# Kernel optimization log

Measured on AMD Instinct MI355X. Metric: run time of the kernel, lower is better.

## Reference

```python
import jax, jax.numpy as jnp
import numpy as np

D_MODEL = 1024
NUM_HEADS = 16
HEAD_DIM = D_MODEL // NUM_HEADS
NUM_KERNELS = 21


def tisa_bias(amp, off, sharp, seq_len):
    # amp/off/sharp: (H, K). Returns (H, L, L) translation-invariant bias.
    # Evaluate on the 2L-1 distinct relative distances, then gather (Toeplitz).
    d = jnp.arange(-(seq_len - 1), seq_len, dtype=amp.dtype)  # (2L-1,)
    # (H, K, 2L-1) -> sum over kernels -> (H, 2L-1)
    scores = jnp.sum(
        amp[:, :, None]
        * jnp.exp(-jnp.abs(sharp)[:, :, None] * (d[None, None, :] - off[:, :, None]) ** 2),
        axis=1,
    )
    i = jnp.arange(seq_len)
    rel_idx = i[None, :] - i[:, None] + (seq_len - 1)  # (L, L) in [0, 2L-2]
    return scores[:, rel_idx]  # (H, L, L)


def setup_inputs() -> dict:
    key = jax.random.key(0)
    ks = jax.random.split(key, 9)
    B, L = 4, 1024
    s = 0.02
    return {
        "x_q": jax.random.normal(ks[0], (B, L, D_MODEL), dtype=jnp.float32),
        "x_kv": jax.random.normal(ks[1], (B, L, D_MODEL), dtype=jnp.float32),
        "Wq": jax.random.normal(ks[2], (D_MODEL, D_MODEL), dtype=jnp.float32) * s,
        "Wm": jax.random.normal(ks[3], (D_MODEL, 2 * D_MODEL), dtype=jnp.float32) * s,
        "Wg": jax.random.normal(ks[4], (D_MODEL, 2 * D_MODEL), dtype=jnp.float32) * s,
        "bg": jnp.zeros((2 * D_MODEL,), dtype=jnp.float32),
        "tisa_amp": jax.random.normal(ks[5], (NUM_HEADS, NUM_KERNELS), dtype=jnp.float32) * 0.1,
        "tisa_off": jax.random.uniform(ks[6], (NUM_HEADS, NUM_KERNELS), dtype=jnp.float32, minval=-512.0, maxval=512.0),
        "tisa_sharp": jax.random.uniform(ks[7], (NUM_HEADS, NUM_KERNELS), dtype=jnp.float32, minval=1e-4, maxval=0.05),
    }


def reference(x_q, x_kv, Wq, Wm, Wg, bg, tisa_amp, tisa_off, tisa_sharp):
    B, Lq, _ = x_q.shape
    Lkv = x_kv.shape[1]
    H, Dh = NUM_HEADS, HEAD_DIM

    q = (x_q @ Wq).reshape(B, Lq, H, Dh).transpose(0, 2, 1, 3)        # (B,H,Lq,Dh)
    mem = (x_kv @ Wm)                                                 # (B,Lkv,2D)
    k = mem[..., :D_MODEL].reshape(B, Lkv, H, Dh).transpose(0, 2, 1, 3)
    v = mem[..., D_MODEL:].reshape(B, Lkv, H, Dh).transpose(0, 2, 1, 3)

    scale = 1.0 / jnp.sqrt(jnp.asarray(Dh, dtype=q.dtype))
    scores = jnp.einsum("bhqd,bhkd->bhqk", q, k) * scale              # (B,H,Lq,Lkv)
    scores = scores + tisa_bias(tisa_amp, tisa_off, tisa_sharp, Lkv)[None]
    weights = jax.nn.softmax(scores, axis=-1)

    attn = jnp.einsum("bhqk,bhkd->bhqd", weights, v)                  # (B,H,Lq,Dh)
    attn = attn.transpose(0, 2, 1, 3).reshape(B, Lq, D_MODEL)

    g = attn @ Wg + bg                                                # (B,Lq,2D)
    a, b = g[..., :D_MODEL], g[..., D_MODEL:]
    return a * jax.nn.sigmoid(b)
```

## Files before the change

kernel.cpp:

```cpp
#include <hip/hip_runtime.h>
#include <cstdint>
#include <cstddef>

typedef __attribute__((ext_vector_type(8))) short bf16x8;
typedef __attribute__((ext_vector_type(4))) float f32x4;

#define LOG2E 1.44269504f

__device__ __forceinline__ unsigned short f2bf(float x) {
  unsigned int u = __float_as_uint(x);
  u += 0x7FFFu + ((u >> 16) & 1u);
  return (unsigned short)(u >> 16);
}
__device__ __forceinline__ unsigned short f2bf_trunc(float x) {
  return (unsigned short)(__float_as_uint(x) >> 16);
}

__device__ __forceinline__ void gload_lds16(const void* g, void* l) {
  __builtin_amdgcn_global_load_lds(
      (const __attribute__((address_space(1))) unsigned int*)g,
      (__attribute__((address_space(3))) unsigned int*)l, 16, 0, 0);
}


__global__ void preproc(const float* __restrict__ x_q, const float* __restrict__ x_kv,
                        const float* __restrict__ Wq, const float* __restrict__ Wm,
                        const float* __restrict__ Wg,
                        const float* __restrict__ amp, const float* __restrict__ off,
                        const float* __restrict__ sharp,
                        ushort4* __restrict__ bXq, ushort4* __restrict__ bXkv,
                        unsigned short* __restrict__ dWq, unsigned short* __restrict__ dWm,
                        unsigned short* __restrict__ dWg, float* __restrict__ tab) {
  __shared__ float tile[32][33];
  const int blk = blockIdx.x;
  if (blk < 8192) {
    int i = blk * 256 + threadIdx.x;
    float4 v;
    ushort4* d;
    if (i < (1 << 20)) { v = ((const float4*)x_q)[i]; d = bXq + i; }
    else { int j = i - (1 << 20); v = ((const float4*)x_kv)[j]; d = bXkv + j; }
    ushort4 o;
    o.x = f2bf(v.x); o.y = f2bf(v.y); o.z = f2bf(v.z); o.w = f2bf(v.w);
    *d = o;
  } else if (blk < 14336) {
    int idx = blk - 8192;
    int z = idx >> 11, rem = idx & 2047;
    int bx = rem & 63, by = rem >> 6;
    const float* src = z == 0 ? Wq : (z == 1 ? Wm : Wg);
    unsigned short* dst = z == 0 ? dWq : (z == 1 ? dWm : dWg);
    int N = z == 0 ? 1024 : 2048;
    int nb = bx * 32, kb = by * 32;
    if (nb >= N) return;
    int tx = threadIdx.x & 31, ty = threadIdx.x >> 5;
#pragma unroll
    for (int r = ty; r < 32; r += 8)
      tile[r][tx] = src[(size_t)(kb + r) * N + nb + tx];
    __syncthreads();
#pragma unroll
    for (int r = ty; r < 32; r += 8)
      dst[(size_t)(nb + r) * 1024 + kb + tx] = f2bf(tile[tx][r]);
  } else {
    int h = blk - 14336;
    for (int idx = threadIdx.x; idx < 2047; idx += 256) {
      float d = (float)(idx - 1023);
      float acc = 0.f;
#pragma unroll
      for (int k = 0; k < 21; ++k) {
        float dd = d - off[h * 21 + k];
        acc += amp[h * 21 + k] * __expf(-fabsf(sharp[h * 21 + k]) * dd * dd);
      }
      tab[h * 2047 + idx] = acc * LOG2E;
    }
  }
}


__global__ __launch_bounds__(512, 2)
void qkv_gemm(const unsigned short* __restrict__ Xq,
              const unsigned short* __restrict__ Xkv,
              const unsigned short* __restrict__ WqT,
              const unsigned short* __restrict__ WmT,
              unsigned short* __restrict__ qbuf,
              unsigned short* __restrict__ kbuf,
              unsigned short* __restrict__ vtbuf) {
  __shared__ unsigned short sA[3][256 * 32];
  __shared__ unsigned short sB[3][256 * 32];
  const int y = blockIdx.y;
  const bool isQ = y < 4;
  const int ntile = (isQ ? y : y - 4) << 8;
  const unsigned short* A = isQ ? Xq : Xkv;
  const unsigned short* Bp = (isQ ? WqT : WmT) + (size_t)ntile * 1024;
  const int mtile = blockIdx.x << 8;
  const int t = threadIdx.x, lane = t & 63, w = t >> 6;
  const int wm = w >> 2, wn = w & 3;
  const int c = lane & 15, g = lane >> 4;

  const int sr = t >> 2;
  const int sch = (t & 3) ^ ((sr >> 1) & 3);
  const unsigned short* aP0 = A + (size_t)(mtile + sr) * 1024 + sch * 8;
  const unsigned short* aP1 = aP0 + 128 * 1024;
  const unsigned short* bP0 = Bp + (size_t)sr * 1024 + sch * 8;
  const unsigned short* bP1 = bP0 + 128 * 1024;
  const int lw = t * 8;

  bf16x8 cur0[4], pend[4], infl[4];
  cur0[0] = *(const bf16x8*)(aP0);
  cur0[1] = *(const bf16x8*)(aP1);
  cur0[2] = *(const bf16x8*)(bP0);
  cur0[3] = *(const bf16x8*)(bP1);
  pend[0] = *(const bf16x8*)(aP0 + 32);
  pend[1] = *(const bf16x8*)(aP1 + 32);
  pend[2] = *(const bf16x8*)(bP0 + 32);
  pend[3] = *(const bf16x8*)(bP1 + 32);
  *(bf16x8*)&sA[0][lw]        = cur0[0];
  *(bf16x8*)&sA[0][4096 + lw] = cur0[1];
  *(bf16x8*)&sB[0][lw]        = cur0[2];
  *(bf16x8*)&sB[0][4096 + lw] = cur0[3];
  asm volatile("s_waitcnt lgkmcnt(0)" ::: "memory");
  __builtin_amdgcn_sched_barrier(0);
  asm volatile("s_barrier" ::: "memory");

  const int gx = (g ^ ((c >> 1) & 3)) * 8;
  const int aoff = (wm * 128 + c) * 32 + gx;
  const int boff = (wn * 64 + c) * 32 + gx;

  f32x4 acc[8][4] = {};
  int s0 = 0, s1 = 1, s2 = 2;

  for (int kt = 0; kt < 32; ++kt) {
    if (kt + 2 < 32) {
      const int ko = (kt + 2) * 32;
      infl[0] = *(const bf16x8*)(aP0 + ko);
      infl[1] = *(const bf16x8*)(aP1 + ko);
      infl[2] = *(const bf16x8*)(bP0 + ko);
      infl[3] = *(const bf16x8*)(bP1 + ko);
    }

    const unsigned short* sAp = &sA[s0][0];
    const unsigned short* sBc = &sB[s0][0];
    bf16x8 bfr[4], a0[4], a1[4];
#pragma unroll
    for (int j = 0; j < 4; ++j) bfr[j] = *(const bf16x8*)&sBc[boff + j * 512];
#pragma unroll
    for (int i = 0; i < 4; ++i) a0[i] = *(const bf16x8*)&sAp[aoff + i * 512];
#pragma unroll
    for (int i = 0; i < 4; ++i) a1[i] = *(const bf16x8*)&sAp[aoff + 2048 + i * 512];

    __builtin_amdgcn_s_setprio(1);
#pragma unroll
    for (int i = 0; i < 4; ++i)
#pragma unroll
      for (int j = 0; j < 4; ++j)
        acc[i][j] = __builtin_amdgcn_mfma_f32_16x16x32_bf16(a0[i], bfr[j], acc[i][j], 0, 0, 0);
#pragma unroll
    for (int i = 0; i < 4; ++i)
#pragma unroll
      for (int j = 0; j < 4; ++j)
        acc[i + 4][j] = __builtin_amdgcn_mfma_f32_16x16x32_bf16(a1[i], bfr[j], acc[i + 4][j], 0, 0, 0);
    __builtin_amdgcn_s_setprio(0);

    if (kt + 1 < 32) {
      *(bf16x8*)&sA[s1][lw]        = pend[0];
      *(bf16x8*)&sA[s1][4096 + lw] = pend[1];
      *(bf16x8*)&sB[s1][lw]        = pend[2];
      *(bf16x8*)&sB[s1][4096 + lw] = pend[3];
    }
#pragma unroll
    for (int q = 0; q < 4; ++q) pend[q] = infl[q];

    asm volatile("s_waitcnt lgkmcnt(0)" ::: "memory");
    __builtin_amdgcn_sched_barrier(0);
    asm volatile("s_barrier" ::: "memory");
    __builtin_amdgcn_sched_barrier(0);

    int tmp = s0; s0 = s1; s1 = s2; s2 = tmp;
  }

  const int row0 = mtile + wm * 128 + (g << 2);
  const int col0 = ntile + wn * 64 + c;
  if (isQ) {
#pragma unroll
    for (int i = 0; i < 8; ++i)
#pragma unroll
      for (int j = 0; j < 4; ++j) {
        int r = row0 + i * 16, cl = col0 + j * 16;
#pragma unroll
        for (int ri = 0; ri < 4; ++ri)
          qbuf[(size_t)(r + ri) * 1024 + cl] = f2bf(acc[i][j][ri] * (0.125f * LOG2E));
      }
  } else if (ntile < 1024) {
#pragma unroll
    for (int i = 0; i < 8; ++i)
#pragma unroll
      for (int j = 0; j < 4; ++j) {
        int r = row0 + i * 16, cl = col0 + j * 16;
#pragma unroll
        for (int ri = 0; ri < 4; ++ri)
          kbuf[(size_t)(r + ri) * 1024 + cl] = f2bf(acc[i][j][ri]);
      }
  } else {
#pragma unroll
    for (int i = 0; i < 8; ++i)
#pragma unroll
      for (int j = 0; j < 4; ++j) {
        int r = row0 + i * 16, cl = col0 + j * 16;
        int d = cl - 1024;
        int hh = d >> 6, dh = d & 63;
        int bb2 = r >> 10, ll = r & 1023;
        ushort4 pk;
        pk.x = f2bf(acc[i][j][0]);
        pk.y = f2bf(acc[i][j][1]);
        pk.z = f2bf(acc[i][j][2]);
        pk.w = f2bf(acc[i][j][3]);
        *(ushort4*)&vtbuf[((size_t)((bb2 * 16 + hh) * 64 + dh) << 10) + ll] = pk;
      }
  }
}


__global__ __launch_bounds__(512)
void attn_kernel(const unsigned short* __restrict__ qbuf,
                 const unsigned short* __restrict__ kbuf,
                 const unsigned short* __restrict__ vtbuf,
                 const float* __restrict__ biasTab,
                 unsigned short* __restrict__ attnb) {
  const int h = blockIdx.x & 15, b = blockIdx.x >> 4, qt = blockIdx.y;
  __shared__ unsigned short sK[2][64 * 64];
  __shared__ unsigned short sV[3][64 * 64];
  __shared__ unsigned short sP[2][128 * 64];
  __shared__ float sLsum[2][128];
  const int t = threadIdx.x, lane = t & 63, w = t >> 6;
  const int c = lane & 15, g = lane >> 4;
  const int rg = w >> 1, cg = w & 1;

  const int r = t >> 3, ch = (t & 7) ^ (r & 7);

  const unsigned short* qsrc = qbuf + (size_t)(b * 1024 + qt * 128) * 1024 + h * 64;
  const unsigned short* ksrc = kbuf + (size_t)(b * 1024) * 1024 + h * 64;
  const unsigned short* vsrc = vtbuf + (size_t)((b * 16 + h) * 64) * 1024;

  unsigned short* sQ = &sP[0][0];
  gload_lds16(qsrc + (size_t)r * 1024 + ch * 8, &sQ[t * 8]);
  gload_lds16(qsrc + (size_t)(r + 64) * 1024 + ch * 8, &sQ[4096 + t * 8]);
  gload_lds16(ksrc + (size_t)r * 1024 + ch * 8, &sK[0][t * 8]);
  gload_lds16(vsrc + (size_t)r * 1024 + ch * 8, &sV[0][t * 8]);

  const float* bb = biasTab + h * 2047 + 1023 + cg * 32 + c - qt * 128 - rg * 32 - g * 4;

  float bc[2][2][4];
#pragma unroll
  for (int rf = 0; rf < 2; ++rf)
#pragma unroll
    for (int nf = 0; nf < 2; ++nf)
#pragma unroll
      for (int ri = 0; ri < 4; ++ri)
        bc[rf][nf][ri] = bb[(nf - rf) * 16 - ri];

  __syncthreads();

  bf16x8 aq[2][2];
#pragma unroll
  for (int rf = 0; rf < 2; ++rf) {
    int row = rg * 32 + rf * 16 + c;
#pragma unroll
    for (int ks = 0; ks < 2; ++ks)
      aq[rf][ks] = *(const bf16x8*)&sQ[row * 64 + (((ks * 4 + g) ^ (row & 7)) * 8)];
  }
  __syncthreads();

  f32x4 o[2][2] = {};
  float lsum[2][4] = {};

  int vcur = 0, vnx = 1;
  for (int kv = 0; kv < 16; ++kv) {
    const int cur = kv & 1;

    f32x4 s[2][2];
#pragma unroll
    for (int rf = 0; rf < 2; ++rf)
#pragma unroll
      for (int nf = 0; nf < 2; ++nf)
#pragma unroll
        for (int ri = 0; ri < 4; ++ri)
          s[rf][nf][ri] = bc[rf][nf][ri];

    if (kv + 1 < 16) {
      gload_lds16(ksrc + (size_t)((kv + 1) * 64 + r) * 1024 + ch * 8, &sK[1 - cur][t * 8]);
      gload_lds16(vsrc + (size_t)r * 1024 + (kv + 1) * 64 + ch * 8, &sV[vnx][t * 8]);
      const float* bk = bb + (kv + 1) * 64;
#pragma unroll
      for (int rf = 0; rf < 2; ++rf)
#pragma unroll
        for (int nf = 0; nf < 2; ++nf)
#pragma unroll
          for (int ri = 0; ri < 4; ++ri)
            bc[rf][nf][ri] = bk[(nf - rf) * 16 - ri];
    }

#pragma unroll
    for (int nf = 0; nf < 2; ++nf) {
      int krow = cg * 32 + nf * 16 + c;
      bf16x8 k0 = *(const bf16x8*)&sK[cur][krow * 64 + (((g) ^ (krow & 7)) * 8)];
      bf16x8 k1 = *(const bf16x8*)&sK[cur][krow * 64 + (((4 + g) ^ (krow & 7)) * 8)];
#pragma unroll
      for (int rf = 0; rf < 2; ++rf) {
        s[rf][nf] = __builtin_amdgcn_mfma_f32_16x16x32_bf16(aq[rf][0], k0, s[rf][nf], 0, 0, 0);
        s[rf][nf] = __builtin_amdgcn_mfma_f32_16x16x32_bf16(aq[rf][1], k1, s[rf][nf], 0, 0, 0);
      }
    }

#pragma unroll
    for (int rf = 0; rf < 2; ++rf)
#pragma unroll
      for (int nf = 0; nf < 2; ++nf)
#pragma unroll
        for (int ri = 0; ri < 4; ++ri) {
          float e = exp2f(s[rf][nf][ri]);
          lsum[rf][ri] += e;
          int prow = rg * 32 + rf * 16 + g * 4 + ri;
          int chunk = cg * 4 + nf * 2 + (c >> 3);
          sP[cur][prow * 64 + ((chunk ^ (prow & 7)) * 8) + (c & 7)] = f2bf_trunc(e);
        }
    __syncthreads();

    bf16x8 ap[2][2];
#pragma unroll
    for (int rf = 0; rf < 2; ++rf) {
      int row = rg * 32 + rf * 16 + c;
#pragma unroll
      for (int ks = 0; ks < 2; ++ks)
        ap[rf][ks] = *(const bf16x8*)&sP[cur][row * 64 + (((ks * 4 + g) ^ (row & 7)) * 8)];
    }
#pragma unroll
    for (int df = 0; df < 2; ++df) {
      int vrow = cg * 32 + df * 16 + c;
      bf16x8 v0 = *(const bf16x8*)&sV[vcur][vrow * 64 + (((g) ^ (vrow & 7)) * 8)];
      bf16x8 v1 = *(const bf16x8*)&sV[vcur][vrow * 64 + (((4 + g) ^ (vrow & 7)) * 8)];
#pragma unroll
      for (int rf = 0; rf < 2; ++rf) {
        o[rf][df] = __builtin_amdgcn_mfma_f32_16x16x32_bf16(ap[rf][0], v0, o[rf][df], 0, 0, 0);
        o[rf][df] = __builtin_amdgcn_mfma_f32_16x16x32_bf16(ap[rf][1], v1, o[rf][df], 0, 0, 0);
      }
    }
    vcur = vnx;
    vnx = (vnx == 2) ? 0 : vnx + 1;
  }

#pragma unroll
  for (int off = 1; off < 16; off <<= 1)
#pragma unroll
    for (int rf = 0; rf < 2; ++rf)
#pragma unroll
      for (int ri = 0; ri < 4; ++ri)
        lsum[rf][ri] += __shfl_xor(lsum[rf][ri], off, 64);
  if (c == 0) {
#pragma unroll
    for (int rf = 0; rf < 2; ++rf)
#pragma unroll
      for (int ri = 0; ri < 4; ++ri)
        sLsum[cg][rg * 32 + rf * 16 + g * 4 + ri] = lsum[rf][ri];
  }
  __syncthreads();

  unsigned short* obase = attnb +
      (size_t)(b * 1024 + qt * 128 + rg * 32 + g * 4) * 1024 + h * 64 + cg * 32 + c;
#pragma unroll
  for (int rf = 0; rf < 2; ++rf)
#pragma unroll
    for (int ri = 0; ri < 4; ++ri) {
      int row = rg * 32 + rf * 16 + g * 4 + ri;
      float rinv = 1.0f / (sLsum[0][row] + sLsum[1][row]);
#pragma unroll
      for (int df = 0; df < 2; ++df)
        obase[(size_t)(rf * 16 + ri) * 1024 + df * 16] = f2bf(o[rf][df][ri] * rinv);
    }
}


__global__ __launch_bounds__(256, 4)
void out_gemm(const unsigned short* __restrict__ A,
              const unsigned short* __restrict__ WgT,
              const float* __restrict__ bg,
              float* __restrict__ out) {
  __shared__ unsigned short sA[2][64 * 32];
  __shared__ unsigned short sB[2][128 * 32];
  const int nb = blockIdx.y;
  const int mtile = blockIdx.x << 6;
  const int t = threadIdx.x, lane = t & 63, w = t >> 6;
  const int c = lane & 15, g = lane >> 4;
  const int rm = w >> 1, cn = w & 1;
  const int srow = t >> 2, scol = (t & 3) << 3;
  const unsigned short* aP = A + (size_t)(mtile + srow) * 1024 + scol;
  const unsigned short* bP0 = WgT + (size_t)(nb * 64 + srow) * 1024 + scol;
  const unsigned short* bP1 = WgT + (size_t)(1024 + nb * 64 + srow) * 1024 + scol;
  const int lo = srow * 32 + scol;

  gload_lds16(aP, &sA[0][lo]);
  gload_lds16(bP0, &sB[0][lo]);
  gload_lds16(bP1, &sB[0][lo + 64 * 32]);
  __syncthreads();

  f32x4 acc[2][4] = {};
  for (int kt = 0; kt < 32; ++kt) {
    const int cur = kt & 1;
    if (kt + 1 < 32) {
      const int ko = (kt + 1) * 32;
      gload_lds16(aP + ko, &sA[1 - cur][lo]);
      gload_lds16(bP0 + ko, &sB[1 - cur][lo]);
      gload_lds16(bP1 + ko, &sB[1 - cur][lo + 64 * 32]);
    }
    bf16x8 af[2], bfr[4];
#pragma unroll
    for (int i = 0; i < 2; ++i)
      af[i] = *(const bf16x8*)&sA[cur][(rm * 32 + i * 16 + c) * 32 + g * 8];
#pragma unroll
    for (int jj = 0; jj < 2; ++jj) {
      bfr[jj]     = *(const bf16x8*)&sB[cur][(cn * 32 + jj * 16 + c) * 32 + g * 8];
      bfr[jj + 2] = *(const bf16x8*)&sB[cur][(64 + cn * 32 + jj * 16 + c) * 32 + g * 8];
    }
#pragma unroll
    for (int i = 0; i < 2; ++i)
#pragma unroll
      for (int j = 0; j < 4; ++j)
        acc[i][j] = __builtin_amdgcn_mfma_f32_16x16x32_bf16(af[i], bfr[j], acc[i][j], 0, 0, 0);
    __syncthreads();
  }

#pragma unroll
  for (int i = 0; i < 2; ++i) {
    int row0 = mtile + rm * 32 + i * 16 + (g << 2);
#pragma unroll
    for (int jj = 0; jj < 2; ++jj) {
      int col = nb * 64 + cn * 32 + jj * 16 + c;
      float ba = bg[col];
      float bbv = bg[1024 + col];
#pragma unroll
      for (int ri = 0; ri < 4; ++ri) {
        float av = acc[i][jj][ri] + ba;
        float bv = acc[i][jj + 2][ri] + bbv;
        out[(size_t)(row0 + ri) * 1024 + col] = av / (1.f + exp2f(-LOG2E * bv));
      }
    }
  }
}


extern "C" void kernel_launch(void* const* d_in, const int* in_sizes, int n_in,
                              void* d_out, int out_size, void* d_ws, size_t ws_size,
                              hipStream_t stream) {
  const float* x_q   = (const float*)d_in[0];
  const float* x_kv  = (const float*)d_in[1];
  const float* Wq    = (const float*)d_in[2];
  const float* Wm    = (const float*)d_in[3];
  const float* Wg    = (const float*)d_in[4];
  const float* bg    = (const float*)d_in[5];
  const float* amp   = (const float*)d_in[6];
  const float* off   = (const float*)d_in[7];
  const float* sharp = (const float*)d_in[8];
  float* out = (float*)d_out;

  char* ws = (char*)d_ws;
  size_t o = 0;
  auto alloc = [&](size_t bytes) {
    char* p = ws + o;
    o += (bytes + 255) & ~(size_t)255;
    return p;
  };
  unsigned short* bXq   = (unsigned short*)alloc(4096ull * 1024 * 2);
  unsigned short* bXkv  = (unsigned short*)alloc(4096ull * 1024 * 2);
  unsigned short* bWqT  = (unsigned short*)alloc(1024ull * 1024 * 2);
  unsigned short* bWmT  = (unsigned short*)alloc(2048ull * 1024 * 2);
  unsigned short* bWgT  = (unsigned short*)alloc(2048ull * 1024 * 2);
  float*          biasT = (float*)alloc(16ull * 2047 * 4);
  unsigned short* qbuf  = (unsigned short*)alloc(4096ull * 1024 * 2);
  unsigned short* kbuf  = (unsigned short*)alloc(4096ull * 1024 * 2);
  unsigned short* vtbuf = (unsigned short*)alloc(4096ull * 1024 * 2);
  unsigned short* attnb = (unsigned short*)alloc(4096ull * 1024 * 2);
  if (ws_size < o) return;

  preproc<<<14352, 256, 0, stream>>>(x_q, x_kv, Wq, Wm, Wg, amp, off, sharp,
                                     (ushort4*)bXq, (ushort4*)bXkv,
                                     bWqT, bWmT, bWgT, biasT);
  qkv_gemm<<<dim3(16, 12), 512, 0, stream>>>(bXq, bXkv, bWqT, bWmT, qbuf, kbuf, vtbuf);
  attn_kernel<<<dim3(64, 8), 512, 0, stream>>>(qbuf, kbuf, vtbuf, biasT, attnb);
  out_gemm<<<dim3(64, 16), 256, 0, stream>>>(attnb, bWgT, bg, out);
}
```

Baseline: 211.6 us.

## Fuse fp32-to-bf16 activation conversion into QKV GEMM loads with 128x128 tiles

Removes the separate pass that converts x_q and x_kv to bf16 in preproc. The QKV GEMM now reads fp32 activations directly and packs them to bf16 before writing to shared memory. The GEMM is also split into two templated launches (Q and KV) with 128x128 tiles, 256 threads and three blocks per SM, replacing the single 256x256 tile kernel. This saves a full write and re-read of the bf16 activation copies, but the GEMM now reads twice the bytes for A and repeats the conversion for every N tile.

After: 220.3 us. 4.1% more time.

```diff
diff --git a/kernel.cpp b/kernel.cpp
--- a/kernel.cpp
+++ b/kernel.cpp
@@ -16,6 +16,15 @@
   return (unsigned short)(__float_as_uint(x) >> 16);
 }
 
+__device__ __forceinline__ bf16x8 pack8(const float4& a, const float4& b) {
+  bf16x8 r;
+  r[0] = (short)f2bf(a.x); r[1] = (short)f2bf(a.y);
+  r[2] = (short)f2bf(a.z); r[3] = (short)f2bf(a.w);
+  r[4] = (short)f2bf(b.x); r[5] = (short)f2bf(b.y);
+  r[6] = (short)f2bf(b.z); r[7] = (short)f2bf(b.w);
+  return r;
+}
+
 __device__ __forceinline__ void gload_lds16(const void* g, void* l) {
   __builtin_amdgcn_global_load_lds(
       (const __attribute__((address_space(1))) unsigned int*)g,
@@ -23,27 +32,16 @@
 }
 
 
-__global__ void preproc(const float* __restrict__ x_q, const float* __restrict__ x_kv,
-                        const float* __restrict__ Wq, const float* __restrict__ Wm,
+__global__ void preproc(const float* __restrict__ Wq, const float* __restrict__ Wm,
                         const float* __restrict__ Wg,
                         const float* __restrict__ amp, const float* __restrict__ off,
                         const float* __restrict__ sharp,
-                        ushort4* __restrict__ bXq, ushort4* __restrict__ bXkv,
                         unsigned short* __restrict__ dWq, unsigned short* __restrict__ dWm,
                         unsigned short* __restrict__ dWg, float* __restrict__ tab) {
   __shared__ float tile[32][33];
   const int blk = blockIdx.x;
-  if (blk < 8192) {
-    int i = blk * 256 + threadIdx.x;
-    float4 v;
-    ushort4* d;
-    if (i < (1 << 20)) { v = ((const float4*)x_q)[i]; d = bXq + i; }
-    else { int j = i - (1 << 20); v = ((const float4*)x_kv)[j]; d = bXkv + j; }
-    ushort4 o;
-    o.x = f2bf(v.x); o.y = f2bf(v.y); o.z = f2bf(v.z); o.w = f2bf(v.w);
-    *d = o;
-  } else if (blk < 14336) {
-    int idx = blk - 8192;
+  if (blk < 6144) {
+    int idx = blk;
     int z = idx >> 11, rem = idx & 2047;
     int bx = rem & 63, by = rem >> 6;
     const float* src = z == 0 ? Wq : (z == 1 ? Wm : Wg);
@@ -60,7 +58,7 @@
     for (int r = ty; r < 32; r += 8)
       dst[(size_t)(nb + r) * 1024 + kb + tx] = f2bf(tile[tx][r]);
   } else {
-    int h = blk - 14336;
+    int h = blk - 6144;
     for (int idx = threadIdx.x; idx < 2047; idx += 256) {
       float d = (float)(idx - 1023);
       float acc = 0.f;
@@ -75,98 +73,94 @@
 }
 
 
-__global__ __launch_bounds__(512, 2)
-void qkv_gemm(const unsigned short* __restrict__ Xq,
-              const unsigned short* __restrict__ Xkv,
-              const unsigned short* __restrict__ WqT,
-              const unsigned short* __restrict__ WmT,
-              unsigned short* __restrict__ qbuf,
-              unsigned short* __restrict__ kbuf,
-              unsigned short* __restrict__ vtbuf) {
-  __shared__ unsigned short sA[3][256 * 32];
-  __shared__ unsigned short sB[3][256 * 32];
-  const int y = blockIdx.y;
-  const bool isQ = y < 4;
-  const int ntile = (isQ ? y : y - 4) << 8;
-  const unsigned short* A = isQ ? Xq : Xkv;
-  const unsigned short* Bp = (isQ ? WqT : WmT) + (size_t)ntile * 1024;
-  const int mtile = blockIdx.x << 8;
+template <int MODE>
+__global__ __launch_bounds__(256, 3)
+void qkv128(const float* __restrict__ X, const unsigned short* __restrict__ WT,
+            unsigned short* __restrict__ qbuf, unsigned short* __restrict__ kbuf,
+            unsigned short* __restrict__ vtbuf) {
+  __shared__ unsigned short sA[3][128 * 32];
+  __shared__ unsigned short sB[3][128 * 32];
+  const int ntile = blockIdx.y << 7;
+  const int mtile = blockIdx.x << 7;
   const int t = threadIdx.x, lane = t & 63, w = t >> 6;
-  const int wm = w >> 2, wn = w & 3;
+  const int wm = w >> 1, wn = w & 1;
   const int c = lane & 15, g = lane >> 4;
 
   const int sr = t >> 2;
   const int sch = (t & 3) ^ ((sr >> 1) & 3);
-  const unsigned short* aP0 = A + (size_t)(mtile + sr) * 1024 + sch * 8;
-  const unsigned short* aP1 = aP0 + 128 * 1024;
-  const unsigned short* bP0 = Bp + (size_t)sr * 1024 + sch * 8;
-  const unsigned short* bP1 = bP0 + 128 * 1024;
+  const float* aP0 = X + (size_t)(mtile + sr) * 1024 + sch * 8;
+  const float* aP1 = aP0 + 64 * 1024;
+  const unsigned short* bP0 = WT + (size_t)(ntile + sr) * 1024 + sch * 8;
+  const unsigned short* bP1 = bP0 + 64 * 1024;
   const int lw = t * 8;
 
-  bf16x8 cur0[4], pend[4], infl[4];
-  cur0[0] = *(const bf16x8*)(aP0);
-  cur0[1] = *(const bf16x8*)(aP1);
-  cur0[2] = *(const bf16x8*)(bP0);
-  cur0[3] = *(const bf16x8*)(bP1);
-  pend[0] = *(const bf16x8*)(aP0 + 32);
-  pend[1] = *(const bf16x8*)(aP1 + 32);
-  pend[2] = *(const bf16x8*)(bP0 + 32);
-  pend[3] = *(const bf16x8*)(bP1 + 32);
-  *(bf16x8*)&sA[0][lw]        = cur0[0];
-  *(bf16x8*)&sA[0][4096 + lw] = cur0[1];
-  *(bf16x8*)&sB[0][lw]        = cur0[2];
-  *(bf16x8*)&sB[0][4096 + lw] = cur0[3];
+  float4 pA[4], iA[4];
+  bf16x8 pB[2], iB[2];
+  {
+    float4 c0 = *(const float4*)(aP0);
+    float4 c1 = *(const float4*)(aP0 + 4);
+    float4 c2 = *(const float4*)(aP1);
+    float4 c3 = *(const float4*)(aP1 + 4);
+    bf16x8 cB0 = *(const bf16x8*)(bP0);
+    bf16x8 cB1 = *(const bf16x8*)(bP1);
+    pA[0] = *(const float4*)(aP0 + 32);
+    pA[1] = *(const float4*)(aP0 + 36);
+    pA[2] = *(const float4*)(aP1 + 32);
+    pA[3] = *(const float4*)(aP1 + 36);
+    pB[0] = *(const bf16x8*)(bP0 + 32);
+    pB[1] = *(const bf16x8*)(bP1 + 32);
+    *(bf16x8*)&sA[0][lw]        = pack8(c0, c1);
+    *(bf16x8*)&sA[0][2048 + lw] = pack8(c2, c3);
+    *(bf16x8*)&sB[0][lw]        = cB0;
+    *(bf16x8*)&sB[0][2048 + lw] = cB1;
+  }
   asm volatile("s_waitcnt lgkmcnt(0)" ::: "memory");
   __builtin_amdgcn_sched_barrier(0);
   asm volatile("s_barrier" ::: "memory");
 
   const int gx = (g ^ ((c >> 1) & 3)) * 8;
-  const int aoff = (wm * 128 + c) * 32 + gx;
+  const int aoff = (wm * 64 + c) * 32 + gx;
   const int boff = (wn * 64 + c) * 32 + gx;
 
-  f32x4 acc[8][4] = {};
+  f32x4 acc[4][4] = {};
   int s0 = 0, s1 = 1, s2 = 2;
 
   for (int kt = 0; kt < 32; ++kt) {
     if (kt + 2 < 32) {
       const int ko = (kt + 2) * 32;
-      infl[0] = *(const bf16x8*)(aP0 + ko);
-      infl[1] = *(const bf16x8*)(aP1 + ko);
-      infl[2] = *(const bf16x8*)(bP0 + ko);
-      infl[3] = *(const bf16x8*)(bP1 + ko);
+      iA[0] = *(const float4*)(aP0 + ko);
+      iA[1] = *(const float4*)(aP0 + ko + 4);
+      iA[2] = *(const float4*)(aP1 + ko);
+      iA[3] = *(const float4*)(aP1 + ko + 4);
+      iB[0] = *(const bf16x8*)(bP0 + ko);
+      iB[1] = *(const bf16x8*)(bP1 + ko);
     }
 
     const unsigned short* sAp = &sA[s0][0];
     const unsigned short* sBc = &sB[s0][0];
-    bf16x8 bfr[4], a0[4], a1[4];
+    bf16x8 af[4], bfr[4];
+#pragma unroll
+    for (int i = 0; i < 4; ++i) af[i]  = *(const bf16x8*)&sAp[aoff + i * 512];
 #pragma unroll
     for (int j = 0; j < 4; ++j) bfr[j] = *(const bf16x8*)&sBc[boff + j * 512];
-#pragma unroll
-    for (int i = 0; i < 4; ++i) a0[i] = *(const bf16x8*)&sAp[aoff + i * 512];
-#pragma unroll
-    for (int i = 0; i < 4; ++i) a1[i] = *(const bf16x8*)&sAp[aoff + 2048 + i * 512];
 
     __builtin_amdgcn_s_setprio(1);
 #pragma unroll
     for (int i = 0; i < 4; ++i)
 #pragma unroll
       for (int j = 0; j < 4; ++j)
-        acc[i][j] = __builtin_amdgcn_mfma_f32_16x16x32_bf16(a0[i], bfr[j], acc[i][j], 0, 0, 0);
-#pragma unroll
-    for (int i = 0; i < 4; ++i)
-#pragma unroll
-      for (int j = 0; j < 4; ++j)
-        acc[i + 4][j] = __builtin_amdgcn_mfma_f32_16x16x32_bf16(a1[i], bfr[j], acc[i + 4][j], 0, 0, 0);
+        acc[i][j] = __builtin_amdgcn_mfma_f32_16x16x32_bf16(af[i], bfr[j], acc[i][j], 0, 0, 0);
     __builtin_amdgcn_s_setprio(0);
 
     if (kt + 1 < 32) {
-      *(bf16x8*)&sA[s1][lw]        = pend[0];
-      *(bf16x8*)&sA[s1][4096 + lw] = pend[1];
-      *(bf16x8*)&sB[s1][lw]        = pend[2];
-      *(bf16x8*)&sB[s1][4096 + lw] = pend[3];
-    }
-#pragma unroll
-    for (int q = 0; q < 4; ++q) pend[q] = infl[q];
+      *(bf16x8*)&sA[s1][lw]        = pack8(pA[0], pA[1]);
+      *(bf16x8*)&sA[s1][2048 + lw] = pack8(pA[2], pA[3]);
+      *(bf16x8*)&sB[s1][lw]        = pB[0];
+      *(bf16x8*)&sB[s1][2048 + lw] = pB[1];
+    }
+#pragma unroll
+    for (int q = 0; q < 4; ++q) pA[q] = iA[q];
+    pB[0] = iB[0]; pB[1] = iB[1];
 
     asm volatile("s_waitcnt lgkmcnt(0)" ::: "memory");
     __builtin_amdgcn_sched_barrier(0);
@@ -176,11 +170,11 @@
     int tmp = s0; s0 = s1; s1 = s2; s2 = tmp;
   }
 
-  const int row0 = mtile + wm * 128 + (g << 2);
+  const int row0 = mtile + wm * 64 + (g << 2);
   const int col0 = ntile + wn * 64 + c;
-  if (isQ) {
-#pragma unroll
-    for (int i = 0; i < 8; ++i)
+  if (MODE == 0) {
+#pragma unroll
+    for (int i = 0; i < 4; ++i)
 #pragma unroll
       for (int j = 0; j < 4; ++j) {
         int r = row0 + i * 16, cl = col0 + j * 16;
@@ -190,7 +184,7 @@
       }
   } else if (ntile < 1024) {
 #pragma unroll
-    for (int i = 0; i < 8; ++i)
+    for (int i = 0; i < 4; ++i)
 #pragma unroll
       for (int j = 0; j < 4; ++j) {
         int r = row0 + i * 16, cl = col0 + j * 16;
@@ -200,7 +194,7 @@
       }
   } else {
 #pragma unroll
-    for (int i = 0; i < 8; ++i)
+    for (int i = 0; i < 4; ++i)
 #pragma unroll
       for (int j = 0; j < 4; ++j) {
         int r = row0 + i * 16, cl = col0 + j * 16;
@@ -466,8 +460,6 @@
     o += (bytes + 255) & ~(size_t)255;
     return p;
   };
-  unsigned short* bXq   = (unsigned short*)alloc(4096ull * 1024 * 2);
-  unsigned short* bXkv  = (unsigned short*)alloc(4096ull * 1024 * 2);
   unsigned short* bWqT  = (unsigned short*)alloc(1024ull * 1024 * 2);
   unsigned short* bWmT  = (unsigned short*)alloc(2048ull * 1024 * 2);
   unsigned short* bWgT  = (unsigned short*)alloc(2048ull * 1024 * 2);
@@ -478,10 +470,10 @@
   unsigned short* attnb = (unsigned short*)alloc(4096ull * 1024 * 2);
   if (ws_size < o) return;
 
-  preproc<<<14352, 256, 0, stream>>>(x_q, x_kv, Wq, Wm, Wg, amp, off, sharp,
-                                     (ushort4*)bXq, (ushort4*)bXkv,
-                                     bWqT, bWmT, bWgT, biasT);
-  qkv_gemm<<<dim3(16, 12), 512, 0, stream>>>(bXq, bXkv, bWqT, bWmT, qbuf, kbuf, vtbuf);
+  preproc<<<6160, 256, 0, stream>>>(Wq, Wm, Wg, amp, off, sharp,
+                                    bWqT, bWmT, bWgT, biasT);
+  qkv128<0><<<dim3(32, 8), 256, 0, stream>>>(x_q, bWqT, qbuf, nullptr, nullptr);
+  qkv128<1><<<dim3(32, 16), 256, 0, stream>>>(x_kv, bWmT, nullptr, kbuf, vtbuf);
   attn_kernel<<<dim3(64, 8), 512, 0, stream>>>(qbuf, kbuf, vtbuf, biasT, attnb);
   out_gemm<<<dim3(64, 16), 256, 0, stream>>>(attnb, bWgT, bg, out);
 }
```
